# Performance work log

Hardware: AMD Instinct MI355X
Metric: run time of the kernel (lower is better)

The kernel has to match this reference:

```python
import jax, jax.numpy as jnp
import numpy as np

N_NODES = 20000
N_EDGES = 320000
HID = 128
IN_NODE = 128
IN_EDGE = 128
OUT = 64
N_LAYERS = 5 - 2  # 3 layers
EPS = 1e-5


def _lin_init(k, din, dout):
    return jax.random.normal(k, (din, dout), jnp.float32) * (1.0 / np.sqrt(din))


def setup_inputs() -> dict:
    key = jax.random.key(0)
    ks = jax.random.split(key, 12)
    h = jax.random.normal(ks[0], (N_NODES, IN_NODE), jnp.float32)
    edge_index = jax.random.randint(ks[1], (2, N_EDGES), 0, N_NODES, jnp.int64)
    edge_attr = jax.random.normal(ks[2], (N_EDGES, IN_EDGE), jnp.float32)
    node_emb_W = _lin_init(ks[3], IN_NODE, HID)
    node_emb_b = jnp.zeros((HID,), jnp.float32)
    edge_emb_W = _lin_init(ks[4], IN_EDGE, HID)
    edge_emb_b = jnp.zeros((HID,), jnp.float32)
    # 5 linears (A,B,C,D,E) per layer, stacked: [L, 5, HID, HID]
    layers_W = jax.random.normal(ks[5], (N_LAYERS, 5, HID, HID), jnp.float32) * (1.0 / np.sqrt(HID))
    layers_b = jax.random.normal(ks[6], (N_LAYERS, 5, HID), jnp.float32) * 0.01
    # bn params: index 0 = node BN, index 1 = edge BN
    bn_gamma = jnp.ones((N_LAYERS, 2, HID), jnp.float32)
    bn_beta = jnp.zeros((N_LAYERS, 2, HID), jnp.float32)
    cls_W1 = _lin_init(ks[7], HID, HID)
    cls_b1 = jnp.zeros((HID,), jnp.float32)
    cls_W2 = _lin_init(ks[8], HID, OUT)
    cls_b2 = jnp.zeros((OUT,), jnp.float32)
    return dict(h=h, edge_index=edge_index, edge_attr=edge_attr,
                node_emb_W=node_emb_W, node_emb_b=node_emb_b,
                edge_emb_W=edge_emb_W, edge_emb_b=edge_emb_b,
                layers_W=layers_W, layers_b=layers_b,
                bn_gamma=bn_gamma, bn_beta=bn_beta,
                cls_W1=cls_W1, cls_b1=cls_b1, cls_W2=cls_W2, cls_b2=cls_b2)


def _bn(x, g, b):
    # BatchNorm1d in train mode: batch mean / biased variance per feature
    mu = jnp.mean(x, axis=0)
    var = jnp.mean((x - mu) ** 2, axis=0)
    return g * (x - mu) * jax.lax.rsqrt(var + EPS) + b


def _forward(h, edge_attr, edge_index, node_emb_W, node_emb_b, edge_emb_W,
             edge_emb_b, layers_W, layers_b, bn_gamma, bn_beta,
             cls_W1, cls_b1, cls_W2, cls_b2):
    n = h.shape[0]
    src, dst = edge_index[0], edge_index[1]
    h = h @ node_emb_W + node_emb_b            # [N, HID]
    e = edge_attr @ edge_emb_W + edge_emb_b    # [E, HID]
    for l in range(layers_W.shape[0]):
        W, b = layers_W[l], layers_b[l]
        Ah = h @ W[0] + b[0]
        Bh = h @ W[1] + b[1]
        Ce = e @ W[2] + b[2]
        Dh = h @ W[3] + b[3]
        Eh = h @ W[4] + b[4]
        e_hat = Ce + Dh[dst] + Eh[src]         # [E, HID]
        sigma = jax.nn.sigmoid(e_hat)
        # edge update: BN -> ReLU -> (dropout p=0) -> residual
        e = e + jax.nn.relu(_bn(e_hat, bn_gamma[l, 1], bn_beta[l, 1]))
        # node update: scatter-add of sigma * Bh[src] onto dst
        agg = jax.ops.segment_sum(sigma * Bh[src], dst, num_segments=n)
        h = h + jax.nn.relu(_bn(Ah + agg, bn_gamma[l, 0], bn_beta[l, 0]))
    out = jnp.mean(h, axis=0, keepdims=True)   # [1, HID]
    out = jax.nn.relu(out @ cls_W1 + cls_b1) @ cls_W2 + cls_b2
    return out


def reference(h, edge_index, edge_attr, node_emb_W, node_emb_b, edge_emb_W,
              edge_emb_b, layers_W, layers_b, bn_gamma, bn_beta,
              cls_W1, cls_b1, cls_W2, cls_b2):
    return _forward(h, edge_attr, edge_index, node_emb_W, node_emb_b,
                    edge_emb_W, edge_emb_b, layers_W, layers_b,
                    bn_gamma, bn_beta, cls_W1, cls_b1, cls_W2, cls_b2)
```

## Files before the change

### kernel.cpp

```cpp
#include <hip/hip_runtime.h>
#include <math.h>

#define NN 20000
#define NE 320000
#define NL 3
#define EPSV 1e-5f
#define MAXD 128
#define ASZ 2560
#define WSZ 5120

#define S_ESC  0
#define S_ESH  128
#define S_NSC  256
#define S_NSH  384
#define S_TOTAL 512

typedef __attribute__((ext_vector_type(8))) short bf16x8;
typedef __attribute__((ext_vector_type(4))) float f32x4;

__device__ __forceinline__ float sigf(float x) { return 1.0f / (1.0f + expf(-x)); }
__device__ __forceinline__ float b2f(unsigned short s) { return __uint_as_float((unsigned)s << 16); }
__device__ __forceinline__ unsigned short f2b(float a)
{
  unsigned u = __float_as_uint(a);
  return (unsigned short)((u + 0x7FFFu + ((u >> 16) & 1u)) >> 16);
}

__device__ __forceinline__ void bsplit(float a, unsigned short& h, unsigned short& l)
{
  unsigned u = __float_as_uint(a);
  unsigned rh = (u + 0x7FFFu + ((u >> 16) & 1u)) >> 16;
  h = (unsigned short)rh;
  float hf = __uint_as_float(rh << 16);
  float d = a - hf;
  unsigned v = __float_as_uint(d);
  l = (unsigned short)((v + 0x7FFFu + ((v >> 16) & 1u)) >> 16);
}

__global__ __launch_bounds__(256) void prep_w(const float* __restrict__ src,
                                              unsigned short* __restrict__ dh,
                                              unsigned short* __restrict__ dl, int nmat)
{
  int idx = blockIdx.x * 256 + threadIdx.x;
  if (idx >= nmat * 16384) return;
  int m = idx >> 14, r = idx & 16383, k = r >> 7, c = r & 127;
  unsigned short h, l;
  bsplit(src[idx], h, l);
  long o = ((long)m << 14) + c * 128 + k;
  dh[o] = h; dl[o] = l;
}

__device__ __forceinline__ void loadW(const unsigned short* __restrict__ Wh_g,
                                      const unsigned short* __restrict__ Wl_g,
                                      int k0, int tid, uint4& h0, uint4& h1, uint4& l0, uint4& l1)
{
  int c0 = tid >> 2, g = tid & 3, c1 = c0 + 64;
  h0 = *(const uint4*)(Wh_g + ((long)c0 << 7) + k0 + g * 8);
  h1 = *(const uint4*)(Wh_g + ((long)c1 << 7) + k0 + g * 8);
  l0 = *(const uint4*)(Wl_g + ((long)c0 << 7) + k0 + g * 8);
  l1 = *(const uint4*)(Wl_g + ((long)c1 << 7) + k0 + g * 8);
}
__device__ __forceinline__ void writeW(const uint4& h0, const uint4& h1, const uint4& l0,
                                       const uint4& l1, int tid,
                                       unsigned short* Wh, unsigned short* Wl)
{
  int c0 = tid >> 2, g = tid & 3, c1 = c0 + 64;
  *(uint4*)(Wh + c0 * 40 + g * 8) = h0;
  *(uint4*)(Wh + c1 * 40 + g * 8) = h1;
  *(uint4*)(Wl + c0 * 40 + g * 8) = l0;
  *(uint4*)(Wl + c1 * 40 + g * 8) = l1;
}
__device__ __forceinline__ void loadA_f32(const float* __restrict__ A, long base, int M,
                                          int tid, int k0, float4& a0, float4& a1)
{
  int r0 = tid >> 3, c4 = tid & 7;
  long g0 = base + r0, g1 = g0 + 32;
  a0 = (g0 < M) ? *(const float4*)(A + g0 * 128 + k0 + c4 * 4) : make_float4(0.f, 0.f, 0.f, 0.f);
  a1 = (g1 < M) ? *(const float4*)(A + g1 * 128 + k0 + c4 * 4) : make_float4(0.f, 0.f, 0.f, 0.f);
}
__device__ __forceinline__ void writeA_pair(const float4& a, int row, int c4,
                                            unsigned short* Ah, unsigned short* Al)
{
  unsigned short h0, l0, h1, l1, h2, l2, h3, l3;
  bsplit(a.x, h0, l0); bsplit(a.y, h1, l1); bsplit(a.z, h2, l2); bsplit(a.w, h3, l3);
  *(uint2*)(Ah + row * 40 + c4 * 4) =
      make_uint2((unsigned)h0 | ((unsigned)h1 << 16), (unsigned)h2 | ((unsigned)h3 << 16));
  *(uint2*)(Al + row * 40 + c4 * 4) =
      make_uint2((unsigned)l0 | ((unsigned)l1 << 16), (unsigned)l2 | ((unsigned)l3 << 16));
}

__device__ __forceinline__ void mfma_frags(int lane, int w, f32x4 acc[4][2],
    const unsigned short* Ah, const unsigned short* Al,
    const unsigned short* Wh, const unsigned short* Wl)
{
  int r16 = lane & 15, g8 = lane >> 4;
  bf16x8 ah[4], al[4], wh[2], wl[2];
  #pragma unroll
  for (int rg = 0; rg < 4; ++rg) {
    ah[rg] = *(const bf16x8*)(Ah + (rg * 16 + r16) * 40 + g8 * 8);
    al[rg] = *(const bf16x8*)(Al + (rg * 16 + r16) * 40 + g8 * 8);
  }
  #pragma unroll
  for (int cg = 0; cg < 2; ++cg) {
    int c = w * 32 + cg * 16 + r16;
    wh[cg] = *(const bf16x8*)(Wh + c * 40 + g8 * 8);
    wl[cg] = *(const bf16x8*)(Wl + c * 40 + g8 * 8);
  }
  #pragma unroll
  for (int rg = 0; rg < 4; ++rg)
    #pragma unroll
    for (int cg = 0; cg < 2; ++cg) {
      acc[rg][cg] = __builtin_amdgcn_mfma_f32_16x16x32_bf16(ah[rg], wh[cg], acc[rg][cg], 0, 0, 0);
      acc[rg][cg] = __builtin_amdgcn_mfma_f32_16x16x32_bf16(ah[rg], wl[cg], acc[rg][cg], 0, 0, 0);
      acc[rg][cg] = __builtin_amdgcn_mfma_f32_16x16x32_bf16(al[rg], wh[cg], acc[rg][cg], 0, 0, 0);
    }
}

__device__ __forceinline__ void mfma_frags2(int lane, int w, f32x4 acc[4][2],
    const unsigned short* Ah, const unsigned short* Wh, const unsigned short* Wl)
{
  int r16 = lane & 15, g8 = lane >> 4;
  bf16x8 ah[4], wh[2], wl[2];
  #pragma unroll
  for (int rg = 0; rg < 4; ++rg)
    ah[rg] = *(const bf16x8*)(Ah + (rg * 16 + r16) * 40 + g8 * 8);
  #pragma unroll
  for (int cg = 0; cg < 2; ++cg) {
    int c = w * 32 + cg * 16 + r16;
    wh[cg] = *(const bf16x8*)(Wh + c * 40 + g8 * 8);
    wl[cg] = *(const bf16x8*)(Wl + c * 40 + g8 * 8);
  }
  #pragma unroll
  for (int rg = 0; rg < 4; ++rg)
    #pragma unroll
    for (int cg = 0; cg < 2; ++cg) {
      acc[rg][cg] = __builtin_amdgcn_mfma_f32_16x16x32_bf16(ah[rg], wh[cg], acc[rg][cg], 0, 0, 0);
      acc[rg][cg] = __builtin_amdgcn_mfma_f32_16x16x32_bf16(ah[rg], wl[cg], acc[rg][cg], 0, 0, 0);
    }
}

#define ACC_INIT                          \
  _Pragma("unroll")                       \
  for (int rg = 0; rg < 4; ++rg)          \
    _Pragma("unroll")                     \
    for (int cg = 0; cg < 2; ++cg)        \
      acc[rg][cg] = (f32x4){0.f, 0.f, 0.f, 0.f};

__device__ __forceinline__ void mfma_core_f32(
    const float* __restrict__ A, long base, int M,
    const unsigned short* __restrict__ Wh_g, const unsigned short* __restrict__ Wl_g,
    int tid, f32x4 acc[4][2],
    unsigned short* Ah, unsigned short* Al, unsigned short* Wh, unsigned short* Wl)
{
  int lane = tid & 63, w = tid >> 6;
  int r0 = tid >> 3, c4 = tid & 7;
  ACC_INIT
  float4 a0, a1; uint4 h0, h1, l0, l1;
  loadA_f32(A, base, M, tid, 0, a0, a1);
  loadW(Wh_g, Wl_g, 0, tid, h0, h1, l0, l1);
  writeA_pair(a0, r0, c4, Ah, Al);
  writeA_pair(a1, r0 + 32, c4, Ah, Al);
  writeW(h0, h1, l0, l1, tid, Wh, Wl);
  for (int ks = 0; ks < 4; ++ks) {
    __syncthreads();
    int cb = ks & 1, nb = cb ^ 1;
    if (ks < 3) {
      loadA_f32(A, base, M, tid, 32 * (ks + 1), a0, a1);
      loadW(Wh_g, Wl_g, 32 * (ks + 1), tid, h0, h1, l0, l1);
    }
    mfma_frags(lane, w, acc, Ah + cb * ASZ, Al + cb * ASZ, Wh + cb * WSZ, Wl + cb * WSZ);
    if (ks < 3) {
      writeA_pair(a0, r0, c4, Ah + nb * ASZ, Al + nb * ASZ);
      writeA_pair(a1, r0 + 32, c4, Ah + nb * ASZ, Al + nb * ASZ);
      writeW(h0, h1, l0, l1, tid, Wh + nb * WSZ, Wl + nb * WSZ);
    }
  }
}

__device__ __forceinline__ void mfma_core_f32i(
    const float* __restrict__ A, const int* ridx,
    const unsigned short* __restrict__ Wh_g, const unsigned short* __restrict__ Wl_g,
    int tid, f32x4 acc[4][2],
    unsigned short* Ah, unsigned short* Al, unsigned short* Wh, unsigned short* Wl)
{
  int lane = tid & 63, w = tid >> 6;
  int r0 = tid >> 3, c4 = tid & 7;
  long g0 = ridx[r0], g1 = ridx[r0 + 32];
  ACC_INIT
  float4 a0, a1; uint4 h0, h1, l0, l1;
  a0 = *(const float4*)(A + g0 * 128 + 0 + c4 * 4);
  a1 = *(const float4*)(A + g1 * 128 + 0 + c4 * 4);
  loadW(Wh_g, Wl_g, 0, tid, h0, h1, l0, l1);
  writeA_pair(a0, r0, c4, Ah, Al);
  writeA_pair(a1, r0 + 32, c4, Ah, Al);
  writeW(h0, h1, l0, l1, tid, Wh, Wl);
  for (int ks = 0; ks < 4; ++ks) {
    __syncthreads();
    int cb = ks & 1, nb = cb ^ 1;
    if (ks < 3) {
      int k0 = 32 * (ks + 1);
      a0 = *(const float4*)(A + g0 * 128 + k0 + c4 * 4);
      a1 = *(const float4*)(A + g1 * 128 + k0 + c4 * 4);
      loadW(Wh_g, Wl_g, k0, tid, h0, h1, l0, l1);
    }
    mfma_frags(lane, w, acc, Ah + cb * ASZ, Al + cb * ASZ, Wh + cb * WSZ, Wl + cb * WSZ);
    if (ks < 3) {
      writeA_pair(a0, r0, c4, Ah + nb * ASZ, Al + nb * ASZ);
      writeA_pair(a1, r0 + 32, c4, Ah + nb * ASZ, Al + nb * ASZ);
      writeW(h0, h1, l0, l1, tid, Wh + nb * WSZ, Wl + nb * WSZ);
    }
  }
}

__device__ __forceinline__ void mfma_core_bf16(
    const unsigned short* __restrict__ Abf, long base,
    const unsigned short* __restrict__ Wh_g, const unsigned short* __restrict__ Wl_g,
    int tid, f32x4 acc[4][2],
    unsigned short* Ah, unsigned short* Wh, unsigned short* Wl)
{
  int lane = tid & 63, w = tid >> 6;
  int row = tid >> 2, q = tid & 3;
  ACC_INIT
  uint4 av, h0, h1, l0, l1;
  long gof = (base + row) * 128 + q * 8;
  av = *(const uint4*)(Abf + gof);
  loadW(Wh_g, Wl_g, 0, tid, h0, h1, l0, l1);
  *(uint4*)(Ah + row * 40 + q * 8) = av;
  writeW(h0, h1, l0, l1, tid, Wh, Wl);
  for (int ks = 0; ks < 4; ++ks) {
    __syncthreads();
    int cb = ks & 1, nb = cb ^ 1;
    if (ks < 3) {
      int k0 = 32 * (ks + 1);
      av = *(const uint4*)(Abf + gof + k0);
      loadW(Wh_g, Wl_g, k0, tid, h0, h1, l0, l1);
    }
    mfma_frags2(lane, w, acc, Ah + cb * ASZ, Wh + cb * WSZ, Wl + cb * WSZ);
    if (ks < 3) {
      *(uint4*)(Ah + nb * ASZ + row * 40 + q * 8) = av;
      writeW(h0, h1, l0, l1, tid, Wh + nb * WSZ, Wl + nb * WSZ);
    }
  }
}

template<bool WB>
__device__ __forceinline__ void mfma_core_upd(
    unsigned short* __restrict__ Ebf,
    const unsigned short* __restrict__ EHAT, long base,
    const unsigned short* __restrict__ Wh_g, const unsigned short* __restrict__ Wl_g,
    const float* s_sc, const float* s_sh,
    int tid, f32x4 acc[4][2],
    unsigned short* Ah, unsigned short* Wh, unsigned short* Wl)
{
  int lane = tid & 63, w = tid >> 6;
  int row = tid >> 2, q = tid & 3;
  ACC_INIT
  uint4 ev, hv, h0, h1, l0, l1;
  long grow = (base + row) * 128;

  ev = *(const uint4*)(Ebf + grow + q * 8);
  hv = *(const uint4*)(EHAT + grow + q * 8);
  loadW(Wh_g, Wl_g, 0, tid, h0, h1, l0, l1);

  #pragma unroll 1
  for (int ks = 0; ks < 4; ++ks) {
    int cb = ks & 1;
    int cbase = ks * 32 + q * 8;
    {
      unsigned es[8] = {ev.x & 0xFFFFu, ev.x >> 16, ev.y & 0xFFFFu, ev.y >> 16,
                        ev.z & 0xFFFFu, ev.z >> 16, ev.w & 0xFFFFu, ev.w >> 16};
      unsigned hs[8] = {hv.x & 0xFFFFu, hv.x >> 16, hv.y & 0xFFFFu, hv.y >> 16,
                        hv.z & 0xFFFFu, hv.z >> 16, hv.w & 0xFFFFu, hv.w >> 16};
      unsigned short nv[8];
      #pragma unroll
      for (int i = 0; i < 8; ++i) {
        float v = b2f((unsigned short)es[i]) +
                  fmaxf(fmaf(s_sc[cbase + i], b2f((unsigned short)hs[i]), s_sh[cbase + i]), 0.f);
        nv[i] = f2b(v);
      }
      uint4 nq = make_uint4((unsigned)nv[0] | ((unsigned)nv[1] << 16),
                            (unsigned)nv[2] | ((unsigned)nv[3] << 16),
                            (unsigned)nv[4] | ((unsigned)nv[5] << 16),
                            (unsigned)nv[6] | ((unsigned)nv[7] << 16));
      *(uint4*)(Ah + cb * ASZ + row * 40 + q * 8) = nq;
      if (WB) *(uint4*)(Ebf + grow + cbase) = nq;
      writeW(h0, h1, l0, l1, tid, Wh + cb * WSZ, Wl + cb * WSZ);
    }
    __syncthreads();
    if (ks < 3) {
      int k0 = 32 * (ks + 1);
      ev = *(const uint4*)(Ebf + grow + k0 + q * 8);
      hv = *(const uint4*)(EHAT + grow + k0 + q * 8);
      loadW(Wh_g, Wl_g, k0, tid, h0, h1, l0, l1);
    }
    mfma_frags2(lane, w, acc, Ah + cb * ASZ, Wh + cb * WSZ, Wl + cb * WSZ);
    if (ks < 2) __syncthreads();
  }
}

__device__ __forceinline__ void edge_epilogue(
    f32x4 acc[4][2], const float* __restrict__ bias,
    const int* __restrict__ srcp, const int* __restrict__ dstp,
    const float* __restrict__ Dh, const float* __restrict__ Eh,
    unsigned short* __restrict__ ehat, float* __restrict__ epart, int do_stats,
    long base, int tid)
{
  int lane = tid & 63, w = tid >> 6;
  int r16 = lane & 15, g8 = lane >> 4;
  int colA = w * 32 + r16, colB = colA + 16;
  float bA = bias[colA], bB = bias[colB];
  float s0 = 0.f, s1 = 0.f, q0 = 0.f, q1 = 0.f;
  #pragma unroll
  for (int rg = 0; rg < 4; ++rg)
    #pragma unroll
    for (int j = 0; j < 4; ++j) {
      long erow = base + rg * 16 + g8 * 4 + j;
      int si = srcp[erow], di = dstp[erow];
      const float* dhp = Dh + (long)di * 128;
      const float* ehp = Eh + (long)si * 128;
      float xA = acc[rg][0][j] + bA + dhp[colA] + ehp[colA];
      float xB = acc[rg][1][j] + bB + dhp[colB] + ehp[colB];
      ehat[erow * 128 + colA] = f2b(xA);
      ehat[erow * 128 + colB] = f2b(xB);
      s0 += xA; q0 += xA * xA; s1 += xB; q1 += xB * xB;
    }
  if (do_stats) {
    s0 += __shfl_xor(s0, 16); s0 += __shfl_xor(s0, 32);
    q0 += __shfl_xor(q0, 16); q0 += __shfl_xor(q0, 32);
    s1 += __shfl_xor(s1, 16); s1 += __shfl_xor(s1, 32);
    q1 += __shfl_xor(q1, 16); q1 += __shfl_xor(q1, 32);
    if (g8 == 0) {
      float* bp = epart + (long)blockIdx.x * 256;
      bp[colA] = s0;       bp[128 + colA] = q0;
      bp[colB] = s1;       bp[128 + colB] = q1;
    }
  }
}

__global__ __launch_bounds__(256) void gemm128(
    const float* __restrict__ A, const unsigned short* __restrict__ Wh_g,
    const unsigned short* __restrict__ Wl_g, const float* __restrict__ bias,
    float* __restrict__ C, int M)
{
  __shared__ unsigned short Ah[2 * ASZ], Al[2 * ASZ], Wh[2 * WSZ], Wl[2 * WSZ];
  int tid = threadIdx.x, lane = tid & 63, w = tid >> 6;
  int r16 = lane & 15, g8 = lane >> 4;
  long base = (long)blockIdx.x * 64;
  f32x4 acc[4][2];
  mfma_core_f32(A, base, M, Wh_g, Wl_g, tid, acc, Ah, Al, Wh, Wl);
  #pragma unroll
  for (int cg = 0; cg < 2; ++cg) {
    int col = w * 32 + cg * 16 + r16;
    float b = bias[col];
    #pragma unroll
    for (int rg = 0; rg < 4; ++rg)
      #pragma unroll
      for (int j = 0; j < 4; ++j) {
        long row = base + rg * 16 + g8 * 4 + j;
        if (row < M) C[row * 128 + col] = acc[rg][cg][j] + b;
      }
  }
}

__global__ __launch_bounds__(256) void gemm128s(
    const float* __restrict__ A, const int* __restrict__ rows,
    const unsigned short* __restrict__ Wh_g, const unsigned short* __restrict__ Wl_g,
    const float* __restrict__ bias,
    unsigned short* __restrict__ Cbf)
{
  __shared__ unsigned short Ah[2 * ASZ], Al[2 * ASZ], Wh[2 * WSZ], Wl[2 * WSZ];
  __shared__ int ridx[64];
  int tid = threadIdx.x, lane = tid & 63, w = tid >> 6;
  int r16 = lane & 15, g8 = lane >> 4;
  long base = (long)blockIdx.x * 64;
  if (tid < 64) ridx[tid] = rows[base + tid];
  __syncthreads();
  f32x4 acc[4][2];
  mfma_core_f32i(A, ridx, Wh_g, Wl_g, tid, acc, Ah, Al, Wh, Wl);
  #pragma unroll
  for (int cg = 0; cg < 2; ++cg) {
    int col = w * 32 + cg * 16 + r16;
    float b = bias[col];
    #pragma unroll
    for (int rg = 0; rg < 4; ++rg)
      #pragma unroll
      for (int j = 0; j < 4; ++j) {
        long row = base + rg * 16 + g8 * 4 + j;
        Cbf[row * 128 + col] = f2b(acc[rg][cg][j] + b);
      }
  }
}

__global__ __launch_bounds__(256) void gemm128_x4(
    const float* __restrict__ A, const unsigned short* __restrict__ Wh_l,
    const unsigned short* __restrict__ Wl_l, const float* __restrict__ bl,
    float* __restrict__ o0, float* __restrict__ o1, float* __restrict__ o2,
    float* __restrict__ o3, int M)
{
  __shared__ unsigned short Ah[2 * ASZ], Al[2 * ASZ], Wh[2 * WSZ], Wl[2 * WSZ];
  int y = blockIdx.y;
  int widx = (y < 2) ? y : y + 1;
  const unsigned short* Wh_g = Wh_l + ((long)widx << 14);
  const unsigned short* Wl_g = Wl_l + ((long)widx << 14);
  const float* bias = bl + (long)widx * 128;
  float* C = (y == 0) ? o0 : (y == 1) ? o1 : (y == 2) ? o2 : o3;
  int tid = threadIdx.x, lane = tid & 63, w = tid >> 6;
  int r16 = lane & 15, g8 = lane >> 4;
  long base = (long)blockIdx.x * 64;
  f32x4 acc[4][2];
  mfma_core_f32(A, base, M, Wh_g, Wl_g, tid, acc, Ah, Al, Wh, Wl);
  #pragma unroll
  for (int cg = 0; cg < 2; ++cg) {
    int col = w * 32 + cg * 16 + r16;
    float b = bias[col];
    #pragma unroll
    for (int rg = 0; rg < 4; ++rg)
      #pragma unroll
      for (int j = 0; j < 4; ++j) {
        long row = base + rg * 16 + g8 * 4 + j;
        if (row < M) C[row * 128 + col] = acc[rg][cg][j] + b;
      }
  }
}

__global__ __launch_bounds__(256) void edge_fused0(
    const unsigned short* __restrict__ ebf,
    const unsigned short* __restrict__ Wh_g, const unsigned short* __restrict__ Wl_g,
    const float* __restrict__ bias, const int* __restrict__ srcp, const int* __restrict__ dstp,
    const float* __restrict__ Dh, const float* __restrict__ Eh,
    unsigned short* __restrict__ ehat, float* __restrict__ epart, int do_stats)
{
  __shared__ unsigned short Ah[2 * ASZ], Wh[2 * WSZ], Wl[2 * WSZ];
  int tid = threadIdx.x;
  long base = (long)blockIdx.x * 64;
  f32x4 acc[4][2];
  mfma_core_bf16(ebf, base, Wh_g, Wl_g, tid, acc, Ah, Wh, Wl);
  edge_epilogue(acc, bias, srcp, dstp, Dh, Eh, ehat, epart, do_stats, base, tid);
}

template<bool WB>
__global__ __launch_bounds__(256) void edge_fusedU(
    unsigned short* __restrict__ ebf,
    unsigned short* __restrict__ ehat,
    const float* __restrict__ scale, const float* __restrict__ shift,
    const unsigned short* __restrict__ Wh_g, const unsigned short* __restrict__ Wl_g,
    const float* __restrict__ bias, const int* __restrict__ srcp, const int* __restrict__ dstp,
    const float* __restrict__ Dh, const float* __restrict__ Eh,
    float* __restrict__ epart, int do_stats)
{
  __shared__ unsigned short Ah[2 * ASZ], Wh[2 * WSZ], Wl[2 * WSZ];
  __shared__ float s_sc[128], s_sh[128];
  int tid = threadIdx.x;
  if (tid < 128) { s_sc[tid] = scale[tid]; s_sh[tid] = shift[tid]; }
  __syncthreads();
  long base = (long)blockIdx.x * 64;
  f32x4 acc[4][2];
  mfma_core_upd<WB>(ebf, ehat, base, Wh_g, Wl_g, s_sc, s_sh, tid, acc, Ah, Wh, Wl);
  edge_epilogue(acc, bias, srcp, dstp, Dh, Eh, ehat, epart, do_stats, base, tid);
}

__global__ __launch_bounds__(256) void reduce_part(const float* __restrict__ in,
                                                   float* __restrict__ outp, int groups)
{
  int t = threadIdx.x;
  long base = (long)blockIdx.x * groups * 256;
  float acc = 0.f;
  for (int i = 0; i < groups; ++i) acc += in[base + i * 256 + t];
  outp[(long)blockIdx.x * 256 + t] = acc;
}

__global__ void finalize_bn_p(const float* __restrict__ part, int np, float invn,
                              const float* __restrict__ gamma, const float* __restrict__ beta,
                              float* __restrict__ scale, float* __restrict__ shift)
{
  int c = threadIdx.x;
  float s = 0.f, q = 0.f;
  for (int p = 0; p < np; ++p) {
    s += part[(long)p * 256 + c];
    q += part[(long)p * 256 + 128 + c];
  }
  float mu = s * invn;
  float var = q * invn - mu * mu;
  float sc = gamma[c] * rsqrtf(var + EPSV);
  scale[c] = sc;
  shift[c] = beta[c] - sc * mu;
}

__global__ __launch_bounds__(256) void hist_dst(const int* __restrict__ dst, int* __restrict__ deg)
{
  int e = blockIdx.x * 256 + threadIdx.x;
  if (e < NE) atomicAdd(&deg[dst[e]], 1);
}

__global__ __launch_bounds__(1024) void scan_deg(const int* __restrict__ deg,
                                                 int* __restrict__ rowstart, int* __restrict__ cursor)
{
  __shared__ int wsum[16];
  __shared__ int carry;
  int tid = threadIdx.x, lane = tid & 63, wid = tid >> 6;
  if (tid == 0) carry = 0;
  __syncthreads();
  for (int base = 0; base < NN; base += 1024) {
    int i = base + tid;
    int v = (i < NN) ? deg[i] : 0;
    int x = v;
    #pragma unroll
    for (int off = 1; off < 64; off <<= 1) {
      int y = __shfl_up(x, off, 64);
      if (lane >= off) x += y;
    }
    if (lane == 63) wsum[wid] = x;
    __syncthreads();
    int wpref = 0;
    for (int j = 0; j < wid; ++j) wpref += wsum[j];
    int excl = carry + wpref + x - v;
    if (i < NN) { rowstart[i] = excl; cursor[i] = excl; }
    __syncthreads();
    if (tid == 1023) carry = excl + v;
    __syncthreads();
  }
  if (tid == 0) rowstart[NN] = NE;
}

__global__ __launch_bounds__(256) void fill_csr(const int* __restrict__ dst,
                                                int* __restrict__ cursor, int* __restrict__ elist)
{
  int e = blockIdx.x * 256 + threadIdx.x;
  if (e < NE) {
    int p = atomicAdd(&cursor[dst[e]], 1);
    elist[p] = e;
  }
}

__global__ __launch_bounds__(128) void seg_sort(const int* __restrict__ rowstart,
                                                int* __restrict__ elist)
{
  __shared__ int buf[MAXD];
  __shared__ int srt[MAXD];
  int n = blockIdx.x;
  int s = rowstart[n], t = rowstart[n + 1];
  int deg = t - s;
  if (deg > MAXD) deg = MAXD;
  int tid = threadIdx.x;
  if (tid < deg) buf[tid] = elist[s + tid];
  __syncthreads();
  if (tid < deg) {
    int v = buf[tid], r = 0;
    for (int j = 0; j < deg; ++j) r += (buf[j] < v);
    srt[r] = v;
  }
  __syncthreads();
  if (tid < deg) elist[s + tid] = srt[tid];
}

__global__ __launch_bounds__(256) void perm_edges(const int* __restrict__ elist,
                                                  const int* __restrict__ src,
                                                  const int* __restrict__ dst,
                                                  int* __restrict__ srcp, int* __restrict__ dstp)
{
  int s = blockIdx.x * 256 + threadIdx.x;
  if (s < NE) {
    int e = elist[s];
    srcp[s] = src[e];
    dstp[s] = dst[e];
  }
}

__global__ __launch_bounds__(128) void gather_node(
    const unsigned short* __restrict__ ehat, const float* __restrict__ Bh,
    const int* __restrict__ srcp, const int* __restrict__ rowstart, float* __restrict__ x)
{
  __shared__ int ssrc[MAXD];
  int n = blockIdx.x;
  int s = rowstart[n], t = rowstart[n + 1];
  int deg = t - s;
  int nload = deg < MAXD ? deg : MAXD;
  int tid = threadIdx.x;
  if (tid < nload) ssrc[tid] = srcp[s + tid];
  __syncthreads();
  float acc = 0.f;
  for (int k = 0; k < nload; ++k)
    acc += sigf(b2f(ehat[(long)(s + k) * 128 + tid])) * Bh[(long)ssrc[k] * 128 + tid];
  for (int k = MAXD; k < deg; ++k)
    acc += sigf(b2f(ehat[(long)(s + k) * 128 + tid])) * Bh[(long)srcp[s + k] * 128 + tid];
  x[(long)n * 128 + tid] += acc;
}

__global__ __launch_bounds__(256) void stats128p(const float* __restrict__ x, float* __restrict__ part)
{
  __shared__ float red[8][32][8];
  int tid = threadIdx.x, tx = tid & 31, ty = tid >> 5;
  long rbase = (long)blockIdx.x * 80;
  float a0 = 0, a1 = 0, a2 = 0, a3 = 0, c0 = 0, c1 = 0, c2 = 0, c3 = 0;
  #pragma unroll
  for (int i = 0; i < 10; ++i) {
    long row = rbase + i * 8 + ty;
    float4 v = *(const float4*)(x + row * 128 + tx * 4);
    a0 += v.x; a1 += v.y; a2 += v.z; a3 += v.w;
    c0 += v.x * v.x; c1 += v.y * v.y; c2 += v.z * v.z; c3 += v.w * v.w;
  }
  red[ty][tx][0] = a0; red[ty][tx][1] = a1; red[ty][tx][2] = a2; red[ty][tx][3] = a3;
  red[ty][tx][4] = c0; red[ty][tx][5] = c1; red[ty][tx][6] = c2; red[ty][tx][7] = c3;
  __syncthreads();
  if (ty == 0) {
    float b0 = 0, b1 = 0, b2 = 0, b3 = 0, d0 = 0, d1 = 0, d2 = 0, d3 = 0;
    #pragma unroll
    for (int t = 0; t < 8; ++t) {
      b0 += red[t][tx][0]; b1 += red[t][tx][1]; b2 += red[t][tx][2]; b3 += red[t][tx][3];
      d0 += red[t][tx][4]; d1 += red[t][tx][5]; d2 += red[t][tx][6]; d3 += red[t][tx][7];
    }
    float* bp = part + (long)blockIdx.x * 256;
    bp[tx * 4 + 0] = b0; bp[tx * 4 + 1] = b1; bp[tx * 4 + 2] = b2; bp[tx * 4 + 3] = b3;
    bp[128 + tx * 4 + 0] = d0; bp[128 + tx * 4 + 1] = d1;
    bp[128 + tx * 4 + 2] = d2; bp[128 + tx * 4 + 3] = d3;
  }
}

__global__ __launch_bounds__(256) void pass2(
    float* __restrict__ dsta, const float* __restrict__ xv,
    const float* __restrict__ scale, const float* __restrict__ shift, long n4)
{
  long i = (long)blockIdx.x * 256 + threadIdx.x;
  if (i >= n4) return;
  int c = (int)(i & 31) * 4;
  float4 x = ((const float4*)xv)[i];
  float4 sc = *(const float4*)(scale + c);
  float4 sh = *(const float4*)(shift + c);
  float4 d = ((const float4*)dsta)[i];
  d.x += fmaxf(fmaf(sc.x, x.x, sh.x), 0.f);
  d.y += fmaxf(fmaf(sc.y, x.y, sh.y), 0.f);
  d.z += fmaxf(fmaf(sc.z, x.z, sh.z), 0.f);
  d.w += fmaxf(fmaf(sc.w, x.w, sh.w), 0.f);
  ((float4*)dsta)[i] = d;
}

__global__ __launch_bounds__(256) void colsum_p(const float* __restrict__ h, float* __restrict__ hpart)
{
  __shared__ float red[8][32][4];
  int tid = threadIdx.x, tx = tid & 31, ty = tid >> 5;
  long rbase = (long)blockIdx.x * 80;
  float a0 = 0, a1 = 0, a2 = 0, a3 = 0;
  #pragma unroll
  for (int i = 0; i < 10; ++i) {
    long row = rbase + i * 8 + ty;
    float4 v = *(const float4*)(h + row * 128 + tx * 4);
    a0 += v.x; a1 += v.y; a2 += v.z; a3 += v.w;
  }
  red[ty][tx][0] = a0; red[ty][tx][1] = a1; red[ty][tx][2] = a2; red[ty][tx][3] = a3;
  __syncthreads();
  if (ty == 0) {
    float b0 = 0, b1 = 0, b2 = 0, b3 = 0;
    #pragma unroll
    for (int t = 0; t < 8; ++t) {
      b0 += red[t][tx][0]; b1 += red[t][tx][1]; b2 += red[t][tx][2]; b3 += red[t][tx][3];
    }
    float* bp = hpart + (long)blockIdx.x * 128;
    bp[tx * 4 + 0] = b0; bp[tx * 4 + 1] = b1; bp[tx * 4 + 2] = b2; bp[tx * 4 + 3] = b3;
  }
}

__global__ void cls_head(const float* __restrict__ hpart,
                         const float* __restrict__ W1, const float* __restrict__ b1,
                         const float* __restrict__ W2, const float* __restrict__ b2,
                         float* __restrict__ out)
{
  __shared__ float hm[128];
  __shared__ float r1[128];
  int t = threadIdx.x;
  float s = 0.f;
  for (int p = 0; p < 250; ++p) s += hpart[(long)p * 128 + t];
  hm[t] = s * (1.0f / NN);
  __syncthreads();
  float v = b1[t];
  for (int k = 0; k < 128; ++k) v = fmaf(hm[k], W1[k * 128 + t], v);
  r1[t] = fmaxf(v, 0.f);
  __syncthreads();
  if (t < 64) {
    float o = b2[t];
    for (int k = 0; k < 128; ++k) o = fmaf(r1[k], W2[k * 64 + t], o);
    out[t] = o;
  }
}

extern "C" void kernel_launch(void* const* d_in, const int* in_sizes, int n_in,
                              void* d_out, int out_size, void* d_ws, size_t ws_size,
                              hipStream_t stream)
{
  const float* h_in  = (const float*)d_in[0];
  const int*   ei    = (const int*)d_in[1];
  const float* eattr = (const float*)d_in[2];
  const float* nW    = (const float*)d_in[3];
  const float* nb    = (const float*)d_in[4];
  const float* eW    = (const float*)d_in[5];
  const float* eb    = (const float*)d_in[6];
  const float* LW    = (const float*)d_in[7];
  const float* LB    = (const float*)d_in[8];
  const float* G     = (const float*)d_in[9];
  const float* Bt    = (const float*)d_in[10];
  const float* W1    = (const float*)d_in[11];
  const float* b1    = (const float*)d_in[12];
  const float* W2    = (const float*)d_in[13];
  const float* b2    = (const float*)d_in[14];
  float* out = (float*)d_out;

  float* ws = (float*)d_ws;
  float* f_h     = ws;
  unsigned short* f_ehat = (unsigned short*)(f_h + (long)NN * 128);
  float* f_A     = (float*)(f_ehat + (long)NE * 128);
  float* f_B     = f_A    + (long)NN * 128;
  float* f_D     = f_B    + (long)NN * 128;
  float* f_E     = f_D    + (long)NN * 128;
  float* f_stats = f_E    + (long)NN * 128;
  float* f_npart = f_stats + S_TOTAL;
  float* f_epart = f_npart + 250 * 256;
  float* f_epart2= f_epart + (long)5000 * 256;
  float* f_hpart = f_epart2 + 50 * 256;
  unsigned short* e_bf = (unsigned short*)(f_hpart + 250 * 128);
  int* i_deg      = (int*)(e_bf + (long)NE * 128);
  int* i_rowstart = i_deg + NN;
  int* i_cursor   = i_rowstart + NN + 1;
  int* i_elist    = i_cursor + NN;
  int* i_srcp     = i_elist + NE;
  int* i_dstp     = i_srcp + NE;
  size_t pw_off = ((((char*)(i_dstp + NE)) - (char*)d_ws) + 15) & ~(size_t)15;
  unsigned short* pw_h = (unsigned short*)((char*)d_ws + pw_off);
  unsigned short* pw_l = pw_h + (long)17 * 16384;
  const int* src = ei;
  const int* dst = ei + NE;

  prep_w<<<64, 256, 0, stream>>>(nW, pw_h, pw_l, 1);
  prep_w<<<64, 256, 0, stream>>>(eW, pw_h + 16384, pw_l + 16384, 1);
  prep_w<<<960, 256, 0, stream>>>(LW, pw_h + 2 * 16384, pw_l + 2 * 16384, 15);

  hipMemsetAsync(i_deg, 0, NN * sizeof(int), stream);
  hist_dst<<<(NE + 255) / 256, 256, 0, stream>>>(dst, i_deg);
  scan_deg<<<1, 1024, 0, stream>>>(i_deg, i_rowstart, i_cursor);
  fill_csr<<<(NE + 255) / 256, 256, 0, stream>>>(dst, i_cursor, i_elist);
  seg_sort<<<NN, 128, 0, stream>>>(i_rowstart, i_elist);
  perm_edges<<<(NE + 255) / 256, 256, 0, stream>>>(i_elist, src, dst, i_srcp, i_dstp);

  gemm128<<<313, 256, 0, stream>>>(h_in, pw_h, pw_l, nb, f_h, NN);
  gemm128s<<<5000, 256, 0, stream>>>(eattr, i_elist, pw_h + 16384, pw_l + 16384, eb, e_bf);

  for (int l = 0; l < NL; ++l) {
    const unsigned short* lwh = pw_h + (long)(2 + l * 5) * 16384;
    const unsigned short* lwl = pw_l + (long)(2 + l * 5) * 16384;
    const float* bl = LB + (long)l * 5 * 128;
    int last = (l == NL - 1);

    gemm128_x4<<<dim3(313, 4), 256, 0, stream>>>(f_h, lwh, lwl, bl, f_A, f_B, f_D, f_E, NN);
    if (l == 0)
      edge_fused0<<<5000, 256, 0, stream>>>(e_bf, lwh + 2 * 16384, lwl + 2 * 16384,
                                            bl + 2 * 128, i_srcp, i_dstp, f_D, f_E,
                                            f_ehat, f_epart, 1);
    else if (l == 1)
      edge_fusedU<true><<<5000, 256, 0, stream>>>(e_bf, f_ehat,
                                                  f_stats + S_ESC, f_stats + S_ESH,
                                                  lwh + 2 * 16384, lwl + 2 * 16384, bl + 2 * 128,
                                                  i_srcp, i_dstp, f_D, f_E, f_epart, 1);
    else
      edge_fusedU<false><<<5000, 256, 0, stream>>>(e_bf, f_ehat,
                                                   f_stats + S_ESC, f_stats + S_ESH,
                                                   lwh + 2 * 16384, lwl + 2 * 16384, bl + 2 * 128,
                                                   i_srcp, i_dstp, f_D, f_E, f_epart, 0);
    if (!last) {
      reduce_part<<<50, 256, 0, stream>>>(f_epart, f_epart2, 100);
      finalize_bn_p<<<1, 128, 0, stream>>>(f_epart2, 50, 1.0f / NE,
                                           G + (l * 2 + 1) * 128, Bt + (l * 2 + 1) * 128,
                                           f_stats + S_ESC, f_stats + S_ESH);
    }
    gather_node<<<NN, 128, 0, stream>>>(f_ehat, f_B, i_srcp, i_rowstart, f_A);
    stats128p<<<250, 256, 0, stream>>>(f_A, f_npart);
    finalize_bn_p<<<1, 128, 0, stream>>>(f_npart, 250, 1.0f / NN,
                                         G + (l * 2 + 0) * 128, Bt + (l * 2 + 0) * 128,
                                         f_stats + S_NSC, f_stats + S_NSH);
    pass2<<<2500, 256, 0, stream>>>(f_h, f_A, f_stats + S_NSC, f_stats + S_NSH, (long)NN * 32);
  }

  colsum_p<<<250, 256, 0, stream>>>(f_h, f_hpart);
  cls_head<<<1, 128, 0, stream>>>(f_hpart, W1, b1, W2, b2, out);
}
```

Measured before the change: 941.2 us.

## Load weight MFMA fragments directly from global into registers, drop LDS weight staging

```diff
diff --git a/kernel.cpp b/kernel.cpp
--- a/kernel.cpp
+++ b/kernel.cpp
@@ -7,7 +7,6 @@
 #define EPSV 1e-5f
 #define MAXD 128
 #define ASZ 2560
-#define WSZ 5120
 
 #define S_ESC  0
 #define S_ESH  128
@@ -50,25 +49,17 @@
   dh[o] = h; dl[o] = l;
 }
 
-__device__ __forceinline__ void loadW(const unsigned short* __restrict__ Wh_g,
-                                      const unsigned short* __restrict__ Wl_g,
-                                      int k0, int tid, uint4& h0, uint4& h1, uint4& l0, uint4& l1)
-{
-  int c0 = tid >> 2, g = tid & 3, c1 = c0 + 64;
-  h0 = *(const uint4*)(Wh_g + ((long)c0 << 7) + k0 + g * 8);
-  h1 = *(const uint4*)(Wh_g + ((long)c1 << 7) + k0 + g * 8);
-  l0 = *(const uint4*)(Wl_g + ((long)c0 << 7) + k0 + g * 8);
-  l1 = *(const uint4*)(Wl_g + ((long)c1 << 7) + k0 + g * 8);
-}
-__device__ __forceinline__ void writeW(const uint4& h0, const uint4& h1, const uint4& l0,
-                                       const uint4& l1, int tid,
-                                       unsigned short* Wh, unsigned short* Wl)
-{
-  int c0 = tid >> 2, g = tid & 3, c1 = c0 + 64;
-  *(uint4*)(Wh + c0 * 40 + g * 8) = h0;
-  *(uint4*)(Wh + c1 * 40 + g * 8) = h1;
-  *(uint4*)(Wl + c0 * 40 + g * 8) = l0;
-  *(uint4*)(Wl + c1 * 40 + g * 8) = l1;
+__device__ __forceinline__ void loadWfrags(const unsigned short* __restrict__ Wh_g,
+                                           const unsigned short* __restrict__ Wl_g,
+                                           int k0, int w, int r16, int g8,
+                                           bf16x8& h0, bf16x8& h1, bf16x8& l0, bf16x8& l1)
+{
+  long o0 = (long)(w * 32 + r16) * 128 + k0 + g8 * 8;
+  long o1 = o0 + 16 * 128;
+  h0 = *(const bf16x8*)(Wh_g + o0);
+  h1 = *(const bf16x8*)(Wh_g + o1);
+  l0 = *(const bf16x8*)(Wl_g + o0);
+  l1 = *(const bf16x8*)(Wl_g + o1);
 }
 __device__ __forceinline__ void loadA_f32(const float* __restrict__ A, long base, int M,
                                           int tid, int k0, float4& a0, float4& a1)
@@ -88,55 +79,49 @@
   *(uint2*)(Al + row * 40 + c4 * 4) =
       make_uint2((unsigned)l0 | ((unsigned)l1 << 16), (unsigned)l2 | ((unsigned)l3 << 16));
 }
-
-__device__ __forceinline__ void mfma_frags(int lane, int w, f32x4 acc[4][2],
+__device__ __forceinline__ void writeA_bf(const float4& a, int row, int c4, unsigned short* Ah)
+{
+  *(uint2*)(Ah + row * 40 + c4 * 4) = make_uint2(
+      (unsigned)f2b(a.x) | ((unsigned)f2b(a.y) << 16),
+      (unsigned)f2b(a.z) | ((unsigned)f2b(a.w) << 16));
+}
+
+__device__ __forceinline__ void mfma_frags3r(int r16, int g8, f32x4 acc[4][2],
     const unsigned short* Ah, const unsigned short* Al,
-    const unsigned short* Wh, const unsigned short* Wl)
-{
-  int r16 = lane & 15, g8 = lane >> 4;
-  bf16x8 ah[4], al[4], wh[2], wl[2];
+    bf16x8 wh0, bf16x8 wh1, bf16x8 wl0, bf16x8 wl1)
+{
+  bf16x8 ah[4], al[4];
   #pragma unroll
   for (int rg = 0; rg < 4; ++rg) {
     ah[rg] = *(const bf16x8*)(Ah + (rg * 16 + r16) * 40 + g8 * 8);
     al[rg] = *(const bf16x8*)(Al + (rg * 16 + r16) * 40 + g8 * 8);
   }
   #pragma unroll
-  for (int cg = 0; cg < 2; ++cg) {
-    int c = w * 32 + cg * 16 + r16;
-    wh[cg] = *(const bf16x8*)(Wh + c * 40 + g8 * 8);
-    wl[cg] = *(const bf16x8*)(Wl + c * 40 + g8 * 8);
-  }
-  #pragma unroll
-  for (int rg = 0; rg < 4; ++rg)
-    #pragma unroll
-    for (int cg = 0; cg < 2; ++cg) {
-      acc[rg][cg] = __builtin_amdgcn_mfma_f32_16x16x32_bf16(ah[rg], wh[cg], acc[rg][cg], 0, 0, 0);
-      acc[rg][cg] = __builtin_amdgcn_mfma_f32_16x16x32_bf16(ah[rg], wl[cg], acc[rg][cg], 0, 0, 0);
-      acc[rg][cg] = __builtin_amdgcn_mfma_f32_16x16x32_bf16(al[rg], wh[cg], acc[rg][cg], 0, 0, 0);
-    }
-}
-
-__device__ __forceinline__ void mfma_frags2(int lane, int w, f32x4 acc[4][2],
-    const unsigned short* Ah, const unsigned short* Wh, const unsigned short* Wl)
-{
-  int r16 = lane & 15, g8 = lane >> 4;
-  bf16x8 ah[4], wh[2], wl[2];
+  for (int rg = 0; rg < 4; ++rg) {
+    acc[rg][0] = __builtin_amdgcn_mfma_f32_16x16x32_bf16(ah[rg], wh0, acc[rg][0], 0, 0, 0);
+    acc[rg][0] = __builtin_amdgcn_mfma_f32_16x16x32_bf16(ah[rg], wl0, acc[rg][0], 0, 0, 0);
+    acc[rg][0] = __builtin_amdgcn_mfma_f32_16x16x32_bf16(al[rg], wh0, acc[rg][0], 0, 0, 0);
+    acc[rg][1] = __builtin_amdgcn_mfma_f32_16x16x32_bf16(ah[rg], wh1, acc[rg][1], 0, 0, 0);
+    acc[rg][1] = __builtin_amdgcn_mfma_f32_16x16x32_bf16(ah[rg], wl1, acc[rg][1], 0, 0, 0);
+    acc[rg][1] = __builtin_amdgcn_mfma_f32_16x16x32_bf16(al[rg], wh1, acc[rg][1], 0, 0, 0);
+  }
+}
+
+__device__ __forceinline__ void mfma_frags2r(int r16, int g8, f32x4 acc[4][2],
+    const unsigned short* Ah,
+    bf16x8 wh0, bf16x8 wh1, bf16x8 wl0, bf16x8 wl1)
+{
+  bf16x8 ah[4];
   #pragma unroll
   for (int rg = 0; rg < 4; ++rg)
     ah[rg] = *(const bf16x8*)(Ah + (rg * 16 + r16) * 40 + g8 * 8);
   #pragma unroll
-  for (int cg = 0; cg < 2; ++cg) {
-    int c = w * 32 + cg * 16 + r16;
-    wh[cg] = *(const bf16x8*)(Wh + c * 40 + g8 * 8);
-    wl[cg] = *(const bf16x8*)(Wl + c * 40 + g8 * 8);
-  }
-  #pragma unroll
-  for (int rg = 0; rg < 4; ++rg)
-    #pragma unroll
-    for (int cg = 0; cg < 2; ++cg) {
-      acc[rg][cg] = __builtin_amdgcn_mfma_f32_16x16x32_bf16(ah[rg], wh[cg], acc[rg][cg], 0, 0, 0);
-      acc[rg][cg] = __builtin_amdgcn_mfma_f32_16x16x32_bf16(ah[rg], wl[cg], acc[rg][cg], 0, 0, 0);
-    }
+  for (int rg = 0; rg < 4; ++rg) {
+    acc[rg][0] = __builtin_amdgcn_mfma_f32_16x16x32_bf16(ah[rg], wh0, acc[rg][0], 0, 0, 0);
+    acc[rg][0] = __builtin_amdgcn_mfma_f32_16x16x32_bf16(ah[rg], wl0, acc[rg][0], 0, 0, 0);
+    acc[rg][1] = __builtin_amdgcn_mfma_f32_16x16x32_bf16(ah[rg], wh1, acc[rg][1], 0, 0, 0);
+    acc[rg][1] = __builtin_amdgcn_mfma_f32_16x16x32_bf16(ah[rg], wl1, acc[rg][1], 0, 0, 0);
+  }
 }
 
 #define ACC_INIT                          \
@@ -149,51 +134,49 @@
 __device__ __forceinline__ void mfma_core_f32(
     const float* __restrict__ A, long base, int M,
     const unsigned short* __restrict__ Wh_g, const unsigned short* __restrict__ Wl_g,
-    int tid, f32x4 acc[4][2],
-    unsigned short* Ah, unsigned short* Al, unsigned short* Wh, unsigned short* Wl)
-{
-  int lane = tid & 63, w = tid >> 6;
+    int tid, f32x4 acc[4][2], unsigned short* Ah, unsigned short* Al)
+{
+  int lane = tid & 63, w = tid >> 6, r16 = lane & 15, g8 = lane >> 4;
   int r0 = tid >> 3, c4 = tid & 7;
   ACC_INIT
-  float4 a0, a1; uint4 h0, h1, l0, l1;
+  float4 a0, a1;
+  bf16x8 wc0, wc1, wc2, wc3, wn0, wn1, wn2, wn3;
   loadA_f32(A, base, M, tid, 0, a0, a1);
-  loadW(Wh_g, Wl_g, 0, tid, h0, h1, l0, l1);
+  loadWfrags(Wh_g, Wl_g, 0, w, r16, g8, wc0, wc1, wc2, wc3);
   writeA_pair(a0, r0, c4, Ah, Al);
   writeA_pair(a1, r0 + 32, c4, Ah, Al);
-  writeW(h0, h1, l0, l1, tid, Wh, Wl);
   for (int ks = 0; ks < 4; ++ks) {
     __syncthreads();
     int cb = ks & 1, nb = cb ^ 1;
     if (ks < 3) {
       loadA_f32(A, base, M, tid, 32 * (ks + 1), a0, a1);
-      loadW(Wh_g, Wl_g, 32 * (ks + 1), tid, h0, h1, l0, l1);
-    }
-    mfma_frags(lane, w, acc, Ah + cb * ASZ, Al + cb * ASZ, Wh + cb * WSZ, Wl + cb * WSZ);
+      loadWfrags(Wh_g, Wl_g, 32 * (ks + 1), w, r16, g8, wn0, wn1, wn2, wn3);
+    }
+    mfma_frags3r(r16, g8, acc, Ah + cb * ASZ, Al + cb * ASZ, wc0, wc1, wc2, wc3);
     if (ks < 3) {
       writeA_pair(a0, r0, c4, Ah + nb * ASZ, Al + nb * ASZ);
       writeA_pair(a1, r0 + 32, c4, Ah + nb * ASZ, Al + nb * ASZ);
-      writeW(h0, h1, l0, l1, tid, Wh + nb * WSZ, Wl + nb * WSZ);
-    }
-  }
-}
-
-__device__ __forceinline__ void mfma_core_f32i(
+      wc0 = wn0; wc1 = wn1; wc2 = wn2; wc3 = wn3;
+    }
+  }
+}
+
+__device__ __forceinline__ void mfma_core_bf16i(
     const float* __restrict__ A, const int* ridx,
     const unsigned short* __restrict__ Wh_g, const unsigned short* __restrict__ Wl_g,
-    int tid, f32x4 acc[4][2],
-    unsigned short* Ah, unsigned short* Al, unsigned short* Wh, unsigned short* Wl)
-{
-  int lane = tid & 63, w = tid >> 6;
+    int tid, f32x4 acc[4][2], unsigned short* Ah)
+{
+  int lane = tid & 63, w = tid >> 6, r16 = lane & 15, g8 = lane >> 4;
   int r0 = tid >> 3, c4 = tid & 7;
   long g0 = ridx[r0], g1 = ridx[r0 + 32];
   ACC_INIT
-  float4 a0, a1; uint4 h0, h1, l0, l1;
-  a0 = *(const float4*)(A + g0 * 128 + 0 + c4 * 4);
-  a1 = *(const float4*)(A + g1 * 128 + 0 + c4 * 4);
-  loadW(Wh_g, Wl_g, 0, tid, h0, h1, l0, l1);
-  writeA_pair(a0, r0, c4, Ah, Al);
-  writeA_pair(a1, r0 + 32, c4, Ah, Al);
-  writeW(h0, h1, l0, l1, tid, Wh, Wl);
+  float4 a0, a1;
+  bf16x8 wc0, wc1, wc2, wc3, wn0, wn1, wn2, wn3;
+  a0 = *(const float4*)(A + g0 * 128 + c4 * 4);
+  a1 = *(const float4*)(A + g1 * 128 + c4 * 4);
+  loadWfrags(Wh_g, Wl_g, 0, w, r16, g8, wc0, wc1, wc2, wc3);
+  writeA_bf(a0, r0, c4, Ah);
+  writeA_bf(a1, r0 + 32, c4, Ah);
   for (int ks = 0; ks < 4; ++ks) {
     __syncthreads();
     int cb = ks & 1, nb = cb ^ 1;
@@ -201,13 +184,13 @@
       int k0 = 32 * (ks + 1);
       a0 = *(const float4*)(A + g0 * 128 + k0 + c4 * 4);
       a1 = *(const float4*)(A + g1 * 128 + k0 + c4 * 4);
-      loadW(Wh_g, Wl_g, k0, tid, h0, h1, l0, l1);
-    }
-    mfma_frags(lane, w, acc, Ah + cb * ASZ, Al + cb * ASZ, Wh + cb * WSZ, Wl + cb * WSZ);
+      loadWfrags(Wh_g, Wl_g, k0, w, r16, g8, wn0, wn1, wn2, wn3);
+    }
+    mfma_frags2r(r16, g8, acc, Ah + cb * ASZ, wc0, wc1, wc2, wc3);
     if (ks < 3) {
-      writeA_pair(a0, r0, c4, Ah + nb * ASZ, Al + nb * ASZ);
-      writeA_pair(a1, r0 + 32, c4, Ah + nb * ASZ, Al + nb * ASZ);
-      writeW(h0, h1, l0, l1, tid, Wh + nb * WSZ, Wl + nb * WSZ);
+      writeA_bf(a0, r0, c4, Ah + nb * ASZ);
+      writeA_bf(a1, r0 + 32, c4, Ah + nb * ASZ);
+      wc0 = wn0; wc1 = wn1; wc2 = wn2; wc3 = wn3;
     }
   }
 }
@@ -215,30 +198,29 @@
 __device__ __forceinline__ void mfma_core_bf16(
     const unsigned short* __restrict__ Abf, long base,
     const unsigned short* __restrict__ Wh_g, const unsigned short* __restrict__ Wl_g,
-    int tid, f32x4 acc[4][2],
-    unsigned short* Ah, unsigned short* Wh, unsigned short* Wl)
-{
-  int lane = tid & 63, w = tid >> 6;
+    int tid, f32x4 acc[4][2], unsigned short* Ah)
+{
+  int lane = tid & 63, w = tid >> 6, r16 = lane & 15, g8 = lane >> 4;
   int row = tid >> 2, q = tid & 3;
   ACC_INIT
-  uint4 av, h0, h1, l0, l1;
+  uint4 av;
+  bf16x8 wc0, wc1, wc2, wc3, wn0, wn1, wn2, wn3;
   long gof = (base + row) * 128 + q * 8;
   av = *(const uint4*)(Abf + gof);
-  loadW(Wh_g, Wl_g, 0, tid, h0, h1, l0, l1);
+  loadWfrags(Wh_g, Wl_g, 0, w, r16, g8, wc0, wc1, wc2, wc3);
   *(uint4*)(Ah + row * 40 + q * 8) = av;
-  writeW(h0, h1, l0, l1, tid, Wh, Wl);
   for (int ks = 0; ks < 4; ++ks) {
     __syncthreads();
     int cb = ks & 1, nb = cb ^ 1;
     if (ks < 3) {
       int k0 = 32 * (ks + 1);
       av = *(const uint4*)(Abf + gof + k0);
-      loadW(Wh_g, Wl_g, k0, tid, h0, h1, l0, l1);
-    }
-    mfma_frags2(lane, w, acc, Ah + cb * ASZ, Wh + cb * WSZ, Wl + cb * WSZ);
+      loadWfrags(Wh_g, Wl_g, k0, w, r16, g8, wn0, wn1, wn2, wn3);
+    }
+    mfma_frags2r(r16, g8, acc, Ah + cb * ASZ, wc0, wc1, wc2, wc3);
     if (ks < 3) {
       *(uint4*)(Ah + nb * ASZ + row * 40 + q * 8) = av;
-      writeW(h0, h1, l0, l1, tid, Wh + nb * WSZ, Wl + nb * WSZ);
+      wc0 = wn0; wc1 = wn1; wc2 = wn2; wc3 = wn3;
     }
   }
 }
@@ -249,18 +231,18 @@
     const unsigned short* __restrict__ EHAT, long base,
     const unsigned short* __restrict__ Wh_g, const unsigned short* __restrict__ Wl_g,
     const float* s_sc, const float* s_sh,
-    int tid, f32x4 acc[4][2],
-    unsigned short* Ah, unsigned short* Wh, unsigned short* Wl)
-{
-  int lane = tid & 63, w = tid >> 6;
+    int tid, f32x4 acc[4][2], unsigned short* Ah)
+{
+  int lane = tid & 63, w = tid >> 6, r16 = lane & 15, g8 = lane >> 4;
   int row = tid >> 2, q = tid & 3;
   ACC_INIT
-  uint4 ev, hv, h0, h1, l0, l1;
+  uint4 ev, hv;
+  bf16x8 wc0, wc1, wc2, wc3, wn0, wn1, wn2, wn3;
   long grow = (base + row) * 128;
 
   ev = *(const uint4*)(Ebf + grow + q * 8);
   hv = *(const uint4*)(EHAT + grow + q * 8);
-  loadW(Wh_g, Wl_g, 0, tid, h0, h1, l0, l1);
+  loadWfrags(Wh_g, Wl_g, 0, w, r16, g8, wc0, wc1, wc2, wc3);
 
   #pragma unroll 1
   for (int ks = 0; ks < 4; ++ks) {
@@ -284,16 +266,16 @@
                             (unsigned)nv[6] | ((unsigned)nv[7] << 16));
       *(uint4*)(Ah + cb * ASZ + row * 40 + q * 8) = nq;
       if (WB) *(uint4*)(Ebf + grow + cbase) = nq;
-      writeW(h0, h1, l0, l1, tid, Wh + cb * WSZ, Wl + cb * WSZ);
     }
     __syncthreads();
     if (ks < 3) {
       int k0 = 32 * (ks + 1);
       ev = *(const uint4*)(Ebf + grow + k0 + q * 8);
       hv = *(const uint4*)(EHAT + grow + k0 + q * 8);
-      loadW(Wh_g, Wl_g, k0, tid, h0, h1, l0, l1);
-    }
-    mfma_frags2(lane, w, acc, Ah + cb * ASZ, Wh + cb * WSZ, Wl + cb * WSZ);
+      loadWfrags(Wh_g, Wl_g, k0, w, r16, g8, wn0, wn1, wn2, wn3);
+    }
+    mfma_frags2r(r16, g8, acc, Ah + cb * ASZ, wc0, wc1, wc2, wc3);
+    if (ks < 3) { wc0 = wn0; wc1 = wn1; wc2 = wn2; wc3 = wn3; }
     if (ks < 2) __syncthreads();
   }
 }
@@ -342,12 +324,12 @@
     const unsigned short* __restrict__ Wl_g, const float* __restrict__ bias,
     float* __restrict__ C, int M)
 {
-  __shared__ unsigned short Ah[2 * ASZ], Al[2 * ASZ], Wh[2 * WSZ], Wl[2 * WSZ];
+  __shared__ unsigned short Ah[2 * ASZ], Al[2 * ASZ];
   int tid = threadIdx.x, lane = tid & 63, w = tid >> 6;
   int r16 = lane & 15, g8 = lane >> 4;
   long base = (long)blockIdx.x * 64;
   f32x4 acc[4][2];
-  mfma_core_f32(A, base, M, Wh_g, Wl_g, tid, acc, Ah, Al, Wh, Wl);
+  mfma_core_f32(A, base, M, Wh_g, Wl_g, tid, acc, Ah, Al);
   #pragma unroll
   for (int cg = 0; cg < 2; ++cg) {
     int col = w * 32 + cg * 16 + r16;
@@ -368,7 +350,7 @@
     const float* __restrict__ bias,
     unsigned short* __restrict__ Cbf)
 {
-  __shared__ unsigned short Ah[2 * ASZ], Al[2 * ASZ], Wh[2 * WSZ], Wl[2 * WSZ];
+  __shared__ unsigned short Ah[2 * ASZ];
   __shared__ int ridx[64];
   int tid = threadIdx.x, lane = tid & 63, w = tid >> 6;
   int r16 = lane & 15, g8 = lane >> 4;
@@ -376,7 +358,7 @@
   if (tid < 64) ridx[tid] = rows[base + tid];
   __syncthreads();
   f32x4 acc[4][2];
-  mfma_core_f32i(A, ridx, Wh_g, Wl_g, tid, acc, Ah, Al, Wh, Wl);
+  mfma_core_bf16i(A, ridx, Wh_g, Wl_g, tid, acc, Ah);
   #pragma unroll
   for (int cg = 0; cg < 2; ++cg) {
     int col = w * 32 + cg * 16 + r16;
@@ -397,7 +379,7 @@
     float* __restrict__ o0, float* __restrict__ o1, float* __restrict__ o2,
     float* __restrict__ o3, int M)
 {
-  __shared__ unsigned short Ah[2 * ASZ], Al[2 * ASZ], Wh[2 * WSZ], Wl[2 * WSZ];
+  __shared__ unsigned short Ah[2 * ASZ], Al[2 * ASZ];
   int y = blockIdx.y;
   int widx = (y < 2) ? y : y + 1;
   const unsigned short* Wh_g = Wh_l + ((long)widx << 14);
@@ -408,7 +390,7 @@
   int r16 = lane & 15, g8 = lane >> 4;
   long base = (long)blockIdx.x * 64;
   f32x4 acc[4][2];
-  mfma_core_f32(A, base, M, Wh_g, Wl_g, tid, acc, Ah, Al, Wh, Wl);
+  mfma_core_f32(A, base, M, Wh_g, Wl_g, tid, acc, Ah, Al);
   #pragma unroll
   for (int cg = 0; cg < 2; ++cg) {
     int col = w * 32 + cg * 16 + r16;
@@ -430,11 +412,11 @@
     const float* __restrict__ Dh, const float* __restrict__ Eh,
     unsigned short* __restrict__ ehat, float* __restrict__ epart, int do_stats)
 {
-  __shared__ unsigned short Ah[2 * ASZ], Wh[2 * WSZ], Wl[2 * WSZ];
+  __shared__ unsigned short Ah[2 * ASZ];
   int tid = threadIdx.x;
   long base = (long)blockIdx.x * 64;
   f32x4 acc[4][2];
-  mfma_core_bf16(ebf, base, Wh_g, Wl_g, tid, acc, Ah, Wh, Wl);
+  mfma_core_bf16(ebf, base, Wh_g, Wl_g, tid, acc, Ah);
   edge_epilogue(acc, bias, srcp, dstp, Dh, Eh, ehat, epart, do_stats, base, tid);
 }
 
@@ -448,14 +430,14 @@
     const float* __restrict__ Dh, const float* __restrict__ Eh,
     float* __restrict__ epart, int do_stats)
 {
-  __shared__ unsigned short Ah[2 * ASZ], Wh[2 * WSZ], Wl[2 * WSZ];
+  __shared__ unsigned short Ah[2 * ASZ];
   __shared__ float s_sc[128], s_sh[128];
   int tid = threadIdx.x;
   if (tid < 128) { s_sc[tid] = scale[tid]; s_sh[tid] = shift[tid]; }
   __syncthreads();
   long base = (long)blockIdx.x * 64;
   f32x4 acc[4][2];
-  mfma_core_upd<WB>(ebf, ehat, base, Wh_g, Wl_g, s_sc, s_sh, tid, acc, Ah, Wh, Wl);
+  mfma_core_upd<WB>(ebf, ehat, base, Wh_g, Wl_g, s_sc, s_sh, tid, acc, Ah);
   edge_epilogue(acc, bias, srcp, dstp, Dh, Eh, ehat, epart, do_stats, base, tid);
 }
 
```

New measurement: 949.4 us. About the same (+0.9%).
